# Performance work log

Measured on AMD Instinct MI355X. Metric: run time of the kernel, lower is better.

Reference implementation:

```python
import jax, jax.numpy as jnp
import numpy as np

N, E, F, DIM, BT, RANK = 8192, 32768, 16, 64, 4, 512
EDGE_VARIABLE = 2


def setup_inputs() -> dict:
    key = jax.random.key(0)
    ks = jax.random.split(key, 24)

    def rn(i, shape, s=0.05):
        return jax.random.normal(ks[i], shape, dtype=jnp.float32) * s

    x = jax.random.normal(ks[0], (N, F), dtype=jnp.float32)
    # first feature column is a categorical node-type id (EDGE_VARIABLE == 2)
    x = x.at[:, 0].set(jax.random.randint(ks[1], (N,), 0, 5).astype(jnp.float32))
    edge_index = jax.random.randint(ks[2], (2, E), 0, N, dtype=jnp.int32)
    edge_attr = jax.random.uniform(ks[3], (E, BT), dtype=jnp.float32)
    return {
        'x': x, 'edge_index': edge_index, 'edge_attr': edge_attr,
        'W0': rn(4, (DIM, F)), 'b0': jnp.zeros(DIM, jnp.float32),
        'nnW1': rn(5, (32, BT)), 'nnb1': jnp.zeros(32, jnp.float32),
        'nnW2': rn(6, (DIM * DIM, 32), 0.02), 'nnb2': jnp.zeros(DIM * DIM, jnp.float32),
        'root': rn(7, (DIM, DIM)), 'conv_b': jnp.zeros(DIM, jnp.float32),
        'Wih': rn(8, (3 * DIM, DIM)), 'Whh': rn(9, (3 * DIM, DIM)),
        'bih': jnp.zeros(3 * DIM, jnp.float32), 'bhh': jnp.zeros(3 * DIM, jnp.float32),
        'W1l': rn(10, (BT, DIM)), 'b1l': jnp.zeros(BT, jnp.float32),
        'WUp': rn(11, (DIM, BT)), 'bUp': jnp.zeros(DIM, jnp.float32),
        'WDown': rn(12, (BT, DIM)), 'bDown': jnp.zeros(BT, jnp.float32),
        'U': rn(13, (BT, RANK, DIM)), 'V': rn(14, (BT, DIM, RANK)),
        'weight': rn(15, (1, DIM), 1.0), 'linW': rn(16, (DIM, DIM)), 'linb': jnp.zeros(DIM, jnp.float32),
        'weight_e': rn(17, (1, BT), 1.0), 'linWe': rn(18, (BT, BT)), 'linbe': jnp.zeros(BT, jnp.float32),
    }


def _gru_cell(m, h, Wih, Whh, bih, bhh):
    # torch GRU gate order: reset, update, new
    gi = m @ Wih.T + bih
    gh = h @ Whh.T + bhh
    ir, iz, i_n = jnp.split(gi, 3, axis=-1)
    hr, hz, h_n = jnp.split(gh, 3, axis=-1)
    r = jax.nn.sigmoid(ir + hr)
    z = jax.nn.sigmoid(iz + hz)
    n = jnp.tanh(i_n + r * h_n)
    return (1.0 - z) * n + z * h


def reference(x, edge_index, edge_attr,
              W0, b0, nnW1, nnb1, nnW2, nnb2, root, conv_b,
              Wih, Whh, bih, bhh, W1l, b1l, WUp, bUp, WDown, bDown,
              U, V, weight, linW, linb, weight_e, linWe, linbe):
    n_nodes = x.shape[0]
    src, dst = edge_index[0], edge_index[1]

    out = jax.nn.relu(x @ W0.T + b0)            # [N, DIM]
    h = out

    # mean-aggregation degree (clamped)
    deg = jnp.clip(jax.ops.segment_sum(jnp.ones_like(src, dtype=out.dtype), dst,
                                       num_segments=n_nodes), 1.0)[:, None]

    # edge-conditioned per-edge weight matrices  [E, DIM, DIM]
    We = (jax.nn.relu(edge_attr @ nnW1.T + nnb1) @ nnW2.T + nnb2).reshape(-1, DIM, DIM)

    for _ in range(3):  # 3 message-passing + GRU steps
        msg = jnp.einsum('ei,eio->eo', out[src], We)                 # per-edge matvec
        agg = jax.ops.segment_sum(msg, dst, num_segments=n_nodes) / deg
        m = jax.nn.relu(out @ root + agg + conv_b)                    # NNConv(root + mean msg)
        h = _gru_cell(m, h, Wih, Whh, bih, bhh)
        out = h

    out_edges = jax.nn.relu(out @ W1l.T + b1l)                        # [N, BT]

    # combine node state with upscaled edge-variable state
    ev_mask = (x[:, 0] == EDGE_VARIABLE)
    out_combine = jnp.where(ev_mask[:, None], out_edges @ WUp.T + bUp, out)

    # FGNet factorized (rank-512) bond-type-conditioned message passing
    bond = jnp.argmax(edge_attr, axis=-1)                             # [E]
    oh = jax.nn.one_hot(bond, BT, dtype=out.dtype)                    # [E, BT]
    h_src = out_combine[src]                                          # [E, DIM]
    zf = jnp.einsum('ed,tdr->etr', h_src, V)                          # [E, BT, RANK]
    zsel = jnp.einsum('etr,et->er', zf, oh)                           # select factor by bond type
    me = jnp.einsum('er,et,trd->ed', zsel, oh, U)                     # [E, DIM]
    msg_f = jax.nn.relu(jax.ops.segment_sum(me, dst, num_segments=n_nodes) / deg)
    msg_to_edge = msg_f @ WDown.T + bDown                             # [N, BT]

    out = out + jax.nn.relu((weight * msg_f) @ linW.T + linb)
    out_edges = out_edges + jax.nn.relu((weight_e * msg_to_edge) @ linWe.T + linbe)
    return jax.nn.log_softmax(out_edges, axis=-1)
```

## Files before the change

kernel.cpp:

```cpp
#include <hip/hip_runtime.h>
#include <hip/hip_bf16.h>

#define NN 8192
#define NE 32768
#define FD 16
#define DIM 64
#define BT 4
#define RANK 512

typedef __attribute__((ext_vector_type(8))) short bf16x8;
typedef __attribute__((ext_vector_type(4))) float f32x4;

__device__ inline unsigned short f2bf(float f) {
    union { float f; unsigned u; } c; c.f = f;
    return (unsigned short)((c.u + 0x7fffu + ((c.u >> 16) & 1u)) >> 16);
}
__device__ inline float ubf(unsigned short h) {
    union { unsigned u; float f; } c; c.u = ((unsigned)h) << 16; return c.f;
}
__device__ inline float bflo(unsigned u) { union { unsigned u; float f; } c; c.u = u << 16; return c.f; }
__device__ inline float bfhi(unsigned u) { union { unsigned u; float f; } c; c.u = u & 0xffff0000u; return c.f; }

__global__ __launch_bounds__(256) void k_prep(
    const float* __restrict__ x, const int* __restrict__ ei, const float* __restrict__ ea,
    const float* __restrict__ W0, const float* __restrict__ b0,
    const float* __restrict__ nnW1, const float* __restrict__ nnb1,
    const float* __restrict__ W2, const float* __restrict__ Wih, const float* __restrict__ Whh,
    const float* __restrict__ root, const float* __restrict__ b2,
    const float* __restrict__ U, const float* __restrict__ V,
    float* __restrict__ s, unsigned short* __restrict__ shi, unsigned short* __restrict__ slo,
    float* __restrict__ deg, int* __restrict__ srccnt,
    float* __restrict__ h32, int* __restrict__ bond,
    unsigned short* __restrict__ w2h, unsigned short* __restrict__ w2l,
    unsigned short* __restrict__ wihh, unsigned short* __restrict__ wihl,
    unsigned short* __restrict__ whhh, unsigned short* __restrict__ whhl,
    unsigned short* __restrict__ rth, unsigned short* __restrict__ rtl,
    unsigned short* __restrict__ b2th, unsigned short* __restrict__ b2tl,
    float* __restrict__ M)
{
    int bid = blockIdx.x, tid = threadIdx.x;
    if (bid < 2048) {
        int gid = bid * 256 + tid;
        int n = gid >> 6, d = gid & 63;
        const float4* xr = (const float4*)(x + (size_t)n * FD);
        const float4* wr = (const float4*)(W0 + d * FD);
        float4 x0 = xr[0], x1 = xr[1], x2 = xr[2], x3 = xr[3];
        float4 w0 = wr[0], w1 = wr[1], w2 = wr[2], w3 = wr[3];
        float acc = b0[d]
            + x0.x*w0.x + x0.y*w0.y + x0.z*w0.z + x0.w*w0.w
            + x1.x*w1.x + x1.y*w1.y + x1.z*w1.z + x1.w*w1.w
            + x2.x*w2.x + x2.y*w2.y + x2.z*w2.z + x2.w*w2.w
            + x3.x*w3.x + x3.y*w3.y + x3.z*w3.z + x3.w*w3.w;
        float sv = fmaxf(acc, 0.f);
        s[gid] = sv;
        unsigned short h = f2bf(sv);
        shi[gid] = h; slo[gid] = f2bf(sv - ubf(h));
    } else if (bid < 2176) {
        int e = (bid - 2048) * 256 + tid;
        atomicAdd(&deg[ei[NE + e]], 1.0f);
        atomicAdd(&srccnt[ei[e]], 1);
    } else if (bid < 6272) {
        int e = (bid - 2176) * 8 + (tid >> 5);
        int k = tid & 31;
        float a0 = ea[e * 4 + 0], a1 = ea[e * 4 + 1], a2 = ea[e * 4 + 2], a3 = ea[e * 4 + 3];
        float h = nnb1[k] + a0 * nnW1[k * 4 + 0] + a1 * nnW1[k * 4 + 1]
                          + a2 * nnW1[k * 4 + 2] + a3 * nnW1[k * 4 + 3];
        h32[e * 32 + k] = fmaxf(h, 0.f);
        if (k == 0) {
            int bi = 0; float bv = a0;
            if (a1 > bv) { bv = a1; bi = 1; }
            if (a2 > bv) { bv = a2; bi = 2; }
            if (a3 > bv) { bv = a3; bi = 3; }
            bond[e] = bi;
        }
    } else if (bid < 6784) {
        int gid = (bid - 6272) * 256 + tid;
        int col = gid >> 6, i = gid & 63;
        float v = W2[(size_t)(i * 64 + (col >> 5)) * 32 + (col & 31)];
        unsigned short h = f2bf(v);
        w2h[gid] = h; w2l[gid] = f2bf(v - ubf(h));
    } else if (bid < 6880) {
        int gid = (bid - 6784) * 256 + tid;
        if (gid < 12288) {
            float v = Wih[gid];
            unsigned short h = f2bf(v);
            wihh[gid] = h; wihl[gid] = f2bf(v - ubf(h));
        } else {
            int g = gid - 12288;
            float v = Whh[g];
            unsigned short h = f2bf(v);
            whhh[g] = h; whhl[g] = f2bf(v - ubf(h));
        }
    } else if (bid < 6896) {
        int gid = (bid - 6880) * 256 + tid;
        int o = gid >> 6, i = gid & 63;
        float v = root[i * 64 + o];
        unsigned short h = f2bf(v);
        rth[gid] = h; rtl[gid] = f2bf(v - ubf(h));
    } else if (bid < 6912) {
        int gid = (bid - 6896) * 256 + tid;
        int o = gid >> 6, i = gid & 63;
        float v = b2[i * 64 + o];
        unsigned short h = f2bf(v);
        b2th[gid] = h; b2tl[gid] = f2bf(v - ubf(h));
    } else {
        __shared__ float red[4][64];
        int t = bid - 6912;
        int b = t >> 6, d = t & 63;
        int chunk = tid >> 6, dp = tid & 63;
        const float* Vp = V + ((size_t)b * DIM + d) * RANK;
        const float* Up = U + (size_t)b * RANK * DIM;
        float acc = 0.f;
        for (int r = chunk * 128; r < chunk * 128 + 128; ++r)
            acc += Vp[r] * Up[(size_t)r * DIM + dp];
        red[chunk][dp] = acc;
        __syncthreads();
        if (chunk == 0)
            M[((size_t)b * DIM + d) * DIM + dp] =
                red[0][dp] + red[1][dp] + red[2][dp] + red[3][dp];
    }
}

__global__ __launch_bounds__(1024) void k_scan(const int* __restrict__ cnt,
                                               int* __restrict__ start, int* __restrict__ cursor) {
    __shared__ int ls[1024];
    int tid = threadIdx.x;
    int v[8], tot = 0;
#pragma unroll
    for (int j = 0; j < 8; ++j) { v[j] = cnt[tid * 8 + j]; tot += v[j]; }
    ls[tid] = tot;
    __syncthreads();
    for (int off = 1; off < 1024; off <<= 1) {
        int t = (tid >= off) ? ls[tid - off] : 0;
        __syncthreads();
        ls[tid] += t;
        __syncthreads();
    }
    int run = ls[tid] - tot;
#pragma unroll
    for (int j = 0; j < 8; ++j) {
        start[tid * 8 + j] = run; cursor[tid * 8 + j] = run; run += v[j];
    }
    if (tid == 1023) start[NN] = run;
}

__global__ __launch_bounds__(256) void k_scatter(const int* __restrict__ ei,
                                                 int* __restrict__ cursor, int* __restrict__ eord) {
    int e = blockIdx.x * 256 + threadIdx.x;
    int pos = atomicAdd(&cursor[ei[e]], 1);
    eord[pos] = e;
}

__global__ __launch_bounds__(256) void k_gemm_A(const unsigned short* __restrict__ sh,
                                                const unsigned short* __restrict__ sl,
                                                const unsigned short* __restrict__ wh,
                                                const unsigned short* __restrict__ wl,
                                                const unsigned short* __restrict__ b2th,
                                                const unsigned short* __restrict__ b2tl,
                                                unsigned short* __restrict__ A,
                                                float* __restrict__ cbuf) {
    int tid = threadIdx.x, wid = tid >> 6, lane = tid & 63;
    int lr = lane & 15, kg = lane >> 4;
    if (blockIdx.y == 16) {
        int rbase = blockIdx.x * 128 + wid * 32;
        f32x4 acc[2][4] = {};
#pragma unroll
        for (int kb = 0; kb < 2; ++kb) {
            bf16x8 ah[2], al[2];
#pragma unroll
            for (int mi = 0; mi < 2; ++mi) {
                size_t off = (size_t)(rbase + mi * 16 + lr) * 64 + kb * 32 + kg * 8;
                ah[mi] = *(const bf16x8*)(sh + off);
                al[mi] = *(const bf16x8*)(sl + off);
            }
#pragma unroll
            for (int ni = 0; ni < 4; ++ni) {
                size_t offB = (size_t)(ni * 16 + lr) * 64 + kb * 32 + kg * 8;
                bf16x8 bh = *(const bf16x8*)(b2th + offB);
                bf16x8 bl = *(const bf16x8*)(b2tl + offB);
#pragma unroll
                for (int mi = 0; mi < 2; ++mi) {
                    acc[mi][ni] = __builtin_amdgcn_mfma_f32_16x16x32_bf16(ah[mi], bh, acc[mi][ni], 0, 0, 0);
                    acc[mi][ni] = __builtin_amdgcn_mfma_f32_16x16x32_bf16(ah[mi], bl, acc[mi][ni], 0, 0, 0);
                    acc[mi][ni] = __builtin_amdgcn_mfma_f32_16x16x32_bf16(al[mi], bh, acc[mi][ni], 0, 0, 0);
                }
            }
        }
#pragma unroll
        for (int mi = 0; mi < 2; ++mi)
#pragma unroll
            for (int r = 0; r < 4; ++r)
#pragma unroll
                for (int ni = 0; ni < 4; ++ni)
                    cbuf[(size_t)(rbase + mi * 16 + kg * 4 + r) * 64 + ni * 16 + lr] = acc[mi][ni][r];
        return;
    }
    int mbase = blockIdx.x * 128 + (wid >> 1) * 64;
    int nbase = blockIdx.y * 128 + (wid & 1) * 64;
    f32x4 acc[4][4] = {};
#pragma unroll
    for (int kb = 0; kb < 2; ++kb) {
        bf16x8 ah[4], al[4], bh[4], bl[4];
#pragma unroll
        for (int mi = 0; mi < 4; ++mi) {
            size_t off = (size_t)(mbase + mi * 16 + lr) * 64 + kb * 32 + kg * 8;
            ah[mi] = *(const bf16x8*)(sh + off);
            al[mi] = *(const bf16x8*)(sl + off);
        }
#pragma unroll
        for (int ni = 0; ni < 4; ++ni) {
            size_t off = (size_t)(nbase + ni * 16 + lr) * 64 + kb * 32 + kg * 8;
            bh[ni] = *(const bf16x8*)(wh + off);
            bl[ni] = *(const bf16x8*)(wl + off);
        }
#pragma unroll
        for (int mi = 0; mi < 4; ++mi)
#pragma unroll
            for (int ni = 0; ni < 4; ++ni) {
                acc[mi][ni] = __builtin_amdgcn_mfma_f32_16x16x32_bf16(ah[mi], bh[ni], acc[mi][ni], 0, 0, 0);
                acc[mi][ni] = __builtin_amdgcn_mfma_f32_16x16x32_bf16(ah[mi], bl[ni], acc[mi][ni], 0, 0, 0);
                acc[mi][ni] = __builtin_amdgcn_mfma_f32_16x16x32_bf16(al[mi], bh[ni], acc[mi][ni], 0, 0, 0);
            }
    }
#pragma unroll
    for (int mi = 0; mi < 4; ++mi)
#pragma unroll
        for (int r = 0; r < 4; ++r) {
            size_t row = (size_t)(mbase + mi * 16 + kg * 4 + r) * 2048;
#pragma unroll
            for (int ni = 0; ni < 4; ++ni)
                A[row + nbase + ni * 16 + lr] = f2bf(acc[mi][ni][r]);
        }
}

__global__ __launch_bounds__(256) void k_edge(const int* __restrict__ ei,
                                              const int* __restrict__ startp,
                                              const int* __restrict__ srccnt,
                                              const int* __restrict__ eord,
                                              const float* __restrict__ h32,
                                              const unsigned short* __restrict__ A,
                                              const float* __restrict__ cbuf,
                                              float* __restrict__ agg) {
    int tid = threadIdx.x, wid = tid >> 6, o = tid & 63;
    int n = blockIdx.x * 4 + wid;
    int cnt = srccnt[n];
    if (cnt == 0) return;
    int beg = startp[n];
    float cv = cbuf[(size_t)n * DIM + o];
    const uint4* Ap = (const uint4*)(A + (size_t)n * 2048 + o * 32);
    uint4 a0 = Ap[0], a1 = Ap[1], a2 = Ap[2], a3 = Ap[3];
    for (int i = beg; i < beg + cnt; ++i) {
        int e = eord[i];
        int dst = ei[NE + e];
        const float4* hp = (const float4*)(h32 + (size_t)e * 32);
        float acc = cv;
        float4 hA = hp[0], hB = hp[1];
        acc += hA.x*bflo(a0.x) + hA.y*bfhi(a0.x) + hA.z*bflo(a0.y) + hA.w*bfhi(a0.y)
             + hB.x*bflo(a0.z) + hB.y*bfhi(a0.z) + hB.z*bflo(a0.w) + hB.w*bfhi(a0.w);
        hA = hp[2]; hB = hp[3];
        acc += hA.x*bflo(a1.x) + hA.y*bfhi(a1.x) + hA.z*bflo(a1.y) + hA.w*bfhi(a1.y)
             + hB.x*bflo(a1.z) + hB.y*bfhi(a1.z) + hB.z*bflo(a1.w) + hB.w*bfhi(a1.w);
        hA = hp[4]; hB = hp[5];
        acc += hA.x*bflo(a2.x) + hA.y*bfhi(a2.x) + hA.z*bflo(a2.y) + hA.w*bfhi(a2.y)
             + hB.x*bflo(a2.z) + hB.y*bfhi(a2.z) + hB.z*bflo(a2.w) + hB.w*bfhi(a2.w);
        hA = hp[6]; hB = hp[7];
        acc += hA.x*bflo(a3.x) + hA.y*bfhi(a3.x) + hA.z*bflo(a3.y) + hA.w*bfhi(a3.y)
             + hB.x*bflo(a3.z) + hB.y*bfhi(a3.z) + hB.z*bflo(a3.w) + hB.w*bfhi(a3.w);
        atomicAdd(&agg[(size_t)dst * DIM + o], acc);
    }
}

__global__ __launch_bounds__(256) void k_upd(
    float* __restrict__ s, unsigned short* __restrict__ shi, unsigned short* __restrict__ slo,
    float* __restrict__ agg, const float* __restrict__ deg, const float* __restrict__ conv_b,
    const unsigned short* __restrict__ rth, const unsigned short* __restrict__ rtl,
    const unsigned short* __restrict__ wihh, const unsigned short* __restrict__ wihl,
    const unsigned short* __restrict__ whhh, const unsigned short* __restrict__ whhl,
    const float* __restrict__ bih, const float* __restrict__ bhh,
    const float* __restrict__ x, const float* __restrict__ W1l, const float* __restrict__ b1l,
    const float* __restrict__ WUp, const float* __restrict__ bUp,
    float* __restrict__ oe, float* __restrict__ oc, int last)
{
    __shared__ unsigned short mh_l[16 * 64];
    __shared__ unsigned short ml_l[16 * 64];
    __shared__ float gl[16 * 384];
    __shared__ float oel[64];
    int tid = threadIdx.x;
    int wid = tid >> 6, lane = tid & 63;
    int lr = lane & 15, kg = lane >> 4;
    int m0 = blockIdx.x * 16;

    bf16x8 sa_h[2], sa_l[2];
#pragma unroll
    for (int kb = 0; kb < 2; ++kb) {
        size_t off = (size_t)(m0 + lr) * 64 + kb * 32 + kg * 8;
        sa_h[kb] = *(const bf16x8*)(shi + off);
        sa_l[kb] = *(const bf16x8*)(slo + off);
    }

    f32x4 macc = {};
#pragma unroll
    for (int kb = 0; kb < 2; ++kb) {
        size_t offB = (size_t)(wid * 16 + lr) * 64 + kb * 32 + kg * 8;
        bf16x8 bh = *(const bf16x8*)(rth + offB);
        bf16x8 bl = *(const bf16x8*)(rtl + offB);
        macc = __builtin_amdgcn_mfma_f32_16x16x32_bf16(sa_h[kb], bh, macc, 0, 0, 0);
        macc = __builtin_amdgcn_mfma_f32_16x16x32_bf16(sa_h[kb], bl, macc, 0, 0, 0);
        macc = __builtin_amdgcn_mfma_f32_16x16x32_bf16(sa_l[kb], bh, macc, 0, 0, 0);
    }
#pragma unroll
    for (int r = 0; r < 4; ++r) {
        int row = m0 + kg * 4 + r;
        float inv = 1.f / fmaxf(deg[row], 1.f);
        int col = wid * 16 + lr;
        size_t idx = (size_t)row * 64 + col;
        float v = macc[r] + agg[idx] * inv + conv_b[col];
        agg[idx] = 0.f;
        v = fmaxf(v, 0.f);
        unsigned short h = f2bf(v);
        int loff = (kg * 4 + r) * 64 + col;
        mh_l[loff] = h; ml_l[loff] = f2bf(v - ubf(h));
    }
    __syncthreads();

    bf16x8 ma_h[2], ma_l[2];
#pragma unroll
    for (int kb = 0; kb < 2; ++kb) {
        int loff = lr * 64 + kb * 32 + kg * 8;
        ma_h[kb] = *(const bf16x8*)(mh_l + loff);
        ma_l[kb] = *(const bf16x8*)(ml_l + loff);
    }
    f32x4 gacc[3] = {}, hacc[3] = {};
#pragma unroll
    for (int kb = 0; kb < 2; ++kb)
#pragma unroll
        for (int j = 0; j < 3; ++j) {
            int ni = wid * 3 + j;
            size_t offB = (size_t)(ni * 16 + lr) * 64 + kb * 32 + kg * 8;
            bf16x8 bh = *(const bf16x8*)(wihh + offB);
            bf16x8 bl = *(const bf16x8*)(wihl + offB);
            gacc[j] = __builtin_amdgcn_mfma_f32_16x16x32_bf16(ma_h[kb], bh, gacc[j], 0, 0, 0);
            gacc[j] = __builtin_amdgcn_mfma_f32_16x16x32_bf16(ma_h[kb], bl, gacc[j], 0, 0, 0);
            gacc[j] = __builtin_amdgcn_mfma_f32_16x16x32_bf16(ma_l[kb], bh, gacc[j], 0, 0, 0);
            bf16x8 ch = *(const bf16x8*)(whhh + offB);
            bf16x8 cl = *(const bf16x8*)(whhl + offB);
            hacc[j] = __builtin_amdgcn_mfma_f32_16x16x32_bf16(sa_h[kb], ch, hacc[j], 0, 0, 0);
            hacc[j] = __builtin_amdgcn_mfma_f32_16x16x32_bf16(sa_h[kb], cl, hacc[j], 0, 0, 0);
            hacc[j] = __builtin_amdgcn_mfma_f32_16x16x32_bf16(sa_l[kb], ch, hacc[j], 0, 0, 0);
        }
#pragma unroll
    for (int j = 0; j < 3; ++j)
#pragma unroll
        for (int r = 0; r < 4; ++r) {
            int row = kg * 4 + r;
            int col = (wid * 3 + j) * 16 + lr;
            gl[row * 384 + col] = gacc[j][r];
            gl[row * 384 + 192 + col] = hacc[j][r];
        }
    __syncthreads();

#pragma unroll
    for (int k = 0; k < 4; ++k) {
        int item = tid + k * 256;
        int row = item >> 6, d = item & 63;
        size_t idx = (size_t)(m0 + row) * 64 + d;
        const float* gr = gl + row * 384;
        float ir = gr[d], iz = gr[64 + d], in_ = gr[128 + d];
        float hr_ = gr[192 + d], hz = gr[256 + d], hn = gr[320 + d];
        float hv = s[idx];
        float rg = 1.f / (1.f + expf(-(ir + bih[d] + hr_ + bhh[d])));
        float z  = 1.f / (1.f + expf(-(iz + bih[64 + d] + hz + bhh[64 + d])));
        float nv = tanhf(in_ + bih[128 + d] + rg * (hn + bhh[128 + d]));
        float nh = (1.f - z) * nv + z * hv;
        if (!last) {
            s[idx] = nh;
            unsigned short hb = f2bf(nh);
            shi[idx] = hb; slo[idx] = f2bf(nh - ubf(hb));
        }
        gl[row * 384 + d] = nh;
    }
    if (!last) return;
    __syncthreads();

    {
        int node16 = tid >> 4, j = tid & 15, t = j & 3, q = j >> 2;
        float p = 0.f;
#pragma unroll
        for (int i = 0; i < 16; ++i)
            p += gl[node16 * 384 + q * 16 + i] * W1l[t * 64 + q * 16 + i];
        p += __shfl_xor(p, 4);
        p += __shfl_xor(p, 8);
        if (q == 0) {
            float v = fmaxf(p + b1l[t], 0.f);
            oel[node16 * 4 + t] = v;
            oe[(size_t)(m0 + node16) * 4 + t] = v;
        }
    }
    __syncthreads();
#pragma unroll
    for (int k = 0; k < 4; ++k) {
        int item = tid + k * 256;
        int row = item >> 6, d = item & 63;
        int node = m0 + row;
        float sval = gl[row * 384 + d];
        float ocv;
        if (x[(size_t)node * FD] == 2.0f) {
            ocv = bUp[d];
#pragma unroll
            for (int t = 0; t < 4; ++t) ocv += oel[row * 4 + t] * WUp[d * 4 + t];
        } else {
            ocv = sval;
        }
        oc[(size_t)node * DIM + d] = ocv;
    }
}

__global__ __launch_bounds__(256) void k_fgedge(const int* __restrict__ ei,
                                                const int* __restrict__ bond,
                                                const float* __restrict__ oc,
                                                const float* __restrict__ M,
                                                float* __restrict__ fg_agg) {
    __shared__ float so[4][64];
    int tid = threadIdx.x, w = tid >> 6, lane = tid & 63;
    int e = blockIdx.x * 4 + w;
    int src = ei[e], dst = ei[NE + e];
    int b = bond[e];
    so[w][lane] = oc[(size_t)src * DIM + lane];
    __syncthreads();
    float acc = 0.f;
    const float* Mp = M + b * DIM * DIM;
    for (int d = 0; d < 64; ++d) acc += so[w][d] * Mp[d * 64 + lane];
    atomicAdd(&fg_agg[(size_t)dst * DIM + lane], acc);
}

__global__ __launch_bounds__(256) void k_final(const float* __restrict__ fg_agg,
                                               const float* __restrict__ deg,
                                               const float* __restrict__ oe,
                                               const float* __restrict__ WDown,
                                               const float* __restrict__ bDown,
                                               const float* __restrict__ weight_e,
                                               const float* __restrict__ linWe,
                                               const float* __restrict__ linbe,
                                               float* __restrict__ out) {
    int tid = threadIdx.x, w = tid >> 6, lane = tid & 63;
    int node = blockIdx.x * 4 + w;
    float degc = fmaxf(deg[node], 1.f);
    float mf = fmaxf(fg_agg[(size_t)node * DIM + lane] / degc, 0.f);
    float mte[4];
#pragma unroll
    for (int t = 0; t < 4; ++t) {
        float p = mf * WDown[t * 64 + lane];
#pragma unroll
        for (int off = 32; off; off >>= 1) p += __shfl_xor(p, off);
        mte[t] = p + bDown[t];
    }
    float val[4];
    float mx = -1e30f;
#pragma unroll
    for (int t = 0; t < 4; ++t) {
        float acc = linbe[t];
#pragma unroll
        for (int t2 = 0; t2 < 4; ++t2) acc += weight_e[t2] * mte[t2] * linWe[t * 4 + t2];
        val[t] = oe[(size_t)node * 4 + t] + fmaxf(acc, 0.f);
        mx = fmaxf(mx, val[t]);
    }
    float lse = 0.f;
#pragma unroll
    for (int t = 0; t < 4; ++t) lse += expf(val[t] - mx);
    lse = logf(lse);
    if (lane < 4) out[(size_t)node * 4 + lane] = val[lane] - mx - lse;
}

extern "C" void kernel_launch(void* const* d_in, const int* in_sizes, int n_in,
                              void* d_out, int out_size, void* d_ws, size_t ws_size,
                              hipStream_t stream) {
    const float* x       = (const float*)d_in[0];
    const int*   ei      = (const int*)  d_in[1];
    const float* ea      = (const float*)d_in[2];
    const float* W0      = (const float*)d_in[3];
    const float* b0      = (const float*)d_in[4];
    const float* nnW1    = (const float*)d_in[5];
    const float* nnb1    = (const float*)d_in[6];
    const float* nnW2    = (const float*)d_in[7];
    const float* nnb2    = (const float*)d_in[8];
    const float* root    = (const float*)d_in[9];
    const float* conv_b  = (const float*)d_in[10];
    const float* Wih     = (const float*)d_in[11];
    const float* Whh     = (const float*)d_in[12];
    const float* bih     = (const float*)d_in[13];
    const float* bhh     = (const float*)d_in[14];
    const float* W1l     = (const float*)d_in[15];
    const float* b1l     = (const float*)d_in[16];
    const float* WUp     = (const float*)d_in[17];
    const float* bUp     = (const float*)d_in[18];
    const float* WDown   = (const float*)d_in[19];
    const float* bDown   = (const float*)d_in[20];
    const float* U       = (const float*)d_in[21];
    const float* V       = (const float*)d_in[22];
    const float* weight_e= (const float*)d_in[26];
    const float* linWe   = (const float*)d_in[27];
    const float* linbe   = (const float*)d_in[28];
    float* out = (float*)d_out;

    char* ws = (char*)d_ws;
    size_t off = 0;
    auto alloc = [&](size_t bytes) { size_t o = off; off = (off + bytes + 255) & ~(size_t)255; return o; };
    float* deg    = (float*)(ws + alloc((size_t)NN * 4));
    int*   srccnt = (int*)  (ws + alloc((size_t)NN * 4));
    float* agg    = (float*)(ws + alloc((size_t)NN * DIM * 4));
    float* fg_agg = (float*)(ws + alloc((size_t)NN * DIM * 4));
    float* s      = (float*)(ws + alloc((size_t)NN * DIM * 4));
    unsigned short* shi = (unsigned short*)(ws + alloc((size_t)NN * DIM * 2));
    unsigned short* slo = (unsigned short*)(ws + alloc((size_t)NN * DIM * 2));
    float* cbuf   = (float*)(ws + alloc((size_t)NN * DIM * 4));
    float* h32    = (float*)(ws + alloc((size_t)NE * 32 * 4));
    int*   bond   = (int*)  (ws + alloc((size_t)NE * 4));
    int*   startp = (int*)  (ws + alloc((size_t)(NN + 1) * 4));
    int*   cursor = (int*)  (ws + alloc((size_t)NN * 4));
    int*   eord   = (int*)  (ws + alloc((size_t)NE * 4));
    float* oe     = (float*)(ws + alloc((size_t)NN * 4 * 4));
    float* oc     = (float*)(ws + alloc((size_t)NN * DIM * 4));
    float* Mbuf   = (float*)(ws + alloc((size_t)BT * DIM * DIM * 4));
    unsigned short* w2h = (unsigned short*)(ws + alloc((size_t)2048 * 64 * 2));
    unsigned short* w2l = (unsigned short*)(ws + alloc((size_t)2048 * 64 * 2));
    unsigned short* wihh = (unsigned short*)(ws + alloc((size_t)192 * 64 * 2));
    unsigned short* wihl = (unsigned short*)(ws + alloc((size_t)192 * 64 * 2));
    unsigned short* whhh = (unsigned short*)(ws + alloc((size_t)192 * 64 * 2));
    unsigned short* whhl = (unsigned short*)(ws + alloc((size_t)192 * 64 * 2));
    unsigned short* rth  = (unsigned short*)(ws + alloc((size_t)64 * 64 * 2));
    unsigned short* rtl  = (unsigned short*)(ws + alloc((size_t)64 * 64 * 2));
    unsigned short* b2th = (unsigned short*)(ws + alloc((size_t)64 * 64 * 2));
    unsigned short* b2tl = (unsigned short*)(ws + alloc((size_t)64 * 64 * 2));
    unsigned short* Abuf = (unsigned short*)(ws + alloc((size_t)NN * 2048 * 2));
    (void)n_in; (void)in_sizes; (void)out_size; (void)ws_size;

    hipMemsetAsync(deg, 0, (size_t)2 * NN * 4, stream);
    hipMemsetAsync(agg, 0, (size_t)2 * NN * DIM * 4, stream);

    k_prep<<<7168, 256, 0, stream>>>(x, ei, ea, W0, b0, nnW1, nnb1,
                                     nnW2, Wih, Whh, root, nnb2, U, V,
                                     s, shi, slo, deg, srccnt, h32, bond,
                                     w2h, w2l, wihh, wihl, whhh, whhl,
                                     rth, rtl, b2th, b2tl, Mbuf);
    k_scan<<<1, 1024, 0, stream>>>(srccnt, startp, cursor);
    k_scatter<<<NE / 256, 256, 0, stream>>>(ei, cursor, eord);

    for (int it = 0; it < 3; ++it) {
        k_gemm_A<<<dim3(NN / 128, 17), 256, 0, stream>>>(shi, slo, w2h, w2l, b2th, b2tl,
                                                         Abuf, cbuf);
        k_edge<<<NN / 4, 256, 0, stream>>>(ei, startp, srccnt, eord, h32, Abuf, cbuf, agg);
        k_upd<<<NN / 16, 256, 0, stream>>>(s, shi, slo, agg, deg, conv_b,
                                           rth, rtl, wihh, wihl, whhh, whhl, bih, bhh,
                                           x, W1l, b1l, WUp, bUp, oe, oc, it == 2);
    }

    k_fgedge<<<NE / 4, 256, 0, stream>>>(ei, bond, oc, Mbuf, fg_agg);
    k_final<<<NN / 4, 256, 0, stream>>>(fg_agg, deg, oe, WDown, bDown, weight_e, linWe, linbe, out);
}
```

Measured before the change: 240.0 us.

## Fuse FG edge messaging with final stage via dst-sorted CSR gather

Builds a destination-sorted edge order (a second scan and scatter pass) so the factorized message passing can gather per node instead of scattering with float atomics. The edge kernel and final kernel are merged into one per-node kernel, which removes the fg_agg buffer and its memset. Zeroing of agg moves from a memset into extra k_prep blocks. In exchange, k_scan runs two serial scans, and per-node loops are unbalanced by in-degree.

```diff
diff --git a/kernel.cpp b/kernel.cpp
--- a/kernel.cpp
+++ b/kernel.cpp
@@ -36,7 +36,7 @@
     unsigned short* __restrict__ whhh, unsigned short* __restrict__ whhl,
     unsigned short* __restrict__ rth, unsigned short* __restrict__ rtl,
     unsigned short* __restrict__ b2th, unsigned short* __restrict__ b2tl,
-    float* __restrict__ M)
+    float* __restrict__ M, float* __restrict__ agg)
 {
     int bid = blockIdx.x, tid = threadIdx.x;
     if (bid < 2048) {
@@ -103,7 +103,7 @@
         float v = b2[i * 64 + o];
         unsigned short h = f2bf(v);
         b2th[gid] = h; b2tl[gid] = f2bf(v - ubf(h));
-    } else {
+    } else if (bid < 7168) {
         __shared__ float red[4][64];
         int t = bid - 6912;
         int b = t >> 6, d = t & 63;
@@ -118,37 +118,67 @@
         if (chunk == 0)
             M[((size_t)b * DIM + d) * DIM + dp] =
                 red[0][dp] + red[1][dp] + red[2][dp] + red[3][dp];
+    } else {
+        float4* zp = ((float4*)agg) + (size_t)(bid - 7168) * 4096;
+        for (int j = tid; j < 4096; j += 256)
+            zp[j] = make_float4(0.f, 0.f, 0.f, 0.f);
     }
 }
 
 __global__ __launch_bounds__(1024) void k_scan(const int* __restrict__ cnt,
-                                               int* __restrict__ start, int* __restrict__ cursor) {
+                                               const float* __restrict__ deg,
+                                               int* __restrict__ start, int* __restrict__ cursor,
+                                               int* __restrict__ dstart, int* __restrict__ dcursor) {
     __shared__ int ls[1024];
     int tid = threadIdx.x;
-    int v[8], tot = 0;
-#pragma unroll
-    for (int j = 0; j < 8; ++j) { v[j] = cnt[tid * 8 + j]; tot += v[j]; }
-    ls[tid] = tot;
+    {
+        int v[8], tot = 0;
+#pragma unroll
+        for (int j = 0; j < 8; ++j) { v[j] = cnt[tid * 8 + j]; tot += v[j]; }
+        ls[tid] = tot;
+        __syncthreads();
+        for (int off = 1; off < 1024; off <<= 1) {
+            int t = (tid >= off) ? ls[tid - off] : 0;
+            __syncthreads();
+            ls[tid] += t;
+            __syncthreads();
+        }
+        int run = ls[tid] - tot;
+#pragma unroll
+        for (int j = 0; j < 8; ++j) {
+            start[tid * 8 + j] = run; cursor[tid * 8 + j] = run; run += v[j];
+        }
+        if (tid == 1023) start[NN] = run;
+    }
     __syncthreads();
-    for (int off = 1; off < 1024; off <<= 1) {
-        int t = (tid >= off) ? ls[tid - off] : 0;
+    {
+        int v[8], tot = 0;
+#pragma unroll
+        for (int j = 0; j < 8; ++j) { v[j] = (int)deg[tid * 8 + j]; tot += v[j]; }
+        ls[tid] = tot;
         __syncthreads();
-        ls[tid] += t;
-        __syncthreads();
-    }
-    int run = ls[tid] - tot;
-#pragma unroll
-    for (int j = 0; j < 8; ++j) {
-        start[tid * 8 + j] = run; cursor[tid * 8 + j] = run; run += v[j];
-    }
-    if (tid == 1023) start[NN] = run;
+        for (int off = 1; off < 1024; off <<= 1) {
+            int t = (tid >= off) ? ls[tid - off] : 0;
+            __syncthreads();
+            ls[tid] += t;
+            __syncthreads();
+        }
+        int run = ls[tid] - tot;
+#pragma unroll
+        for (int j = 0; j < 8; ++j) {
+            dstart[tid * 8 + j] = run; dcursor[tid * 8 + j] = run; run += v[j];
+        }
+        if (tid == 1023) dstart[NN] = run;
+    }
 }
 
 __global__ __launch_bounds__(256) void k_scatter(const int* __restrict__ ei,
-                                                 int* __restrict__ cursor, int* __restrict__ eord) {
+                                                 int* __restrict__ cursor, int* __restrict__ eord,
+                                                 int* __restrict__ dcursor, int* __restrict__ eordD) {
     int e = blockIdx.x * 256 + threadIdx.x;
-    int pos = atomicAdd(&cursor[ei[e]], 1);
-    eord[pos] = e;
+    int s_ = ei[e], d_ = ei[NE + e];
+    eord[atomicAdd(&cursor[s_], 1)] = e;
+    eordD[atomicAdd(&dcursor[d_], 1)] = e;
 }
 
 __global__ __launch_bounds__(256) void k_gemm_A(const unsigned short* __restrict__ sh,
@@ -415,37 +445,37 @@
     }
 }
 
-__global__ __launch_bounds__(256) void k_fgedge(const int* __restrict__ ei,
-                                                const int* __restrict__ bond,
-                                                const float* __restrict__ oc,
-                                                const float* __restrict__ M,
-                                                float* __restrict__ fg_agg) {
-    __shared__ float so[4][64];
-    int tid = threadIdx.x, w = tid >> 6, lane = tid & 63;
-    int e = blockIdx.x * 4 + w;
-    int src = ei[e], dst = ei[NE + e];
-    int b = bond[e];
-    so[w][lane] = oc[(size_t)src * DIM + lane];
-    __syncthreads();
+__global__ __launch_bounds__(256) void k_fg(const int* __restrict__ ei,
+                                            const int* __restrict__ bond,
+                                            const int* __restrict__ dstart,
+                                            const int* __restrict__ eordD,
+                                            const float* __restrict__ oc,
+                                            const float* __restrict__ M,
+                                            const float* __restrict__ deg,
+                                            const float* __restrict__ oe,
+                                            const float* __restrict__ WDown,
+                                            const float* __restrict__ bDown,
+                                            const float* __restrict__ weight_e,
+                                            const float* __restrict__ linWe,
+                                            const float* __restrict__ linbe,
+                                            float* __restrict__ out) {
+    int tid = threadIdx.x, wid = tid >> 6, lane = tid & 63;
+    int node = blockIdx.x * 4 + wid;
+    float degf = deg[node];
+    int cnt = (int)degf;
+    int beg = dstart[node];
     float acc = 0.f;
-    const float* Mp = M + b * DIM * DIM;
-    for (int d = 0; d < 64; ++d) acc += so[w][d] * Mp[d * 64 + lane];
-    atomicAdd(&fg_agg[(size_t)dst * DIM + lane], acc);
-}
-
-__global__ __launch_bounds__(256) void k_final(const float* __restrict__ fg_agg,
-                                               const float* __restrict__ deg,
-                                               const float* __restrict__ oe,
-                                               const float* __restrict__ WDown,
-                                               const float* __restrict__ bDown,
-                                               const float* __restrict__ weight_e,
-                                               const float* __restrict__ linWe,
-                                               const float* __restrict__ linbe,
-                                               float* __restrict__ out) {
-    int tid = threadIdx.x, w = tid >> 6, lane = tid & 63;
-    int node = blockIdx.x * 4 + w;
-    float degc = fmaxf(deg[node], 1.f);
-    float mf = fmaxf(fg_agg[(size_t)node * DIM + lane] / degc, 0.f);
+    for (int i = 0; i < cnt; ++i) {
+        int e = eordD[beg + i];
+        int src = ei[e];
+        int b = bond[e];
+        float ocv = oc[(size_t)src * DIM + lane];
+        const float* Mp = M + b * DIM * DIM;
+#pragma unroll
+        for (int d = 0; d < 64; ++d)
+            acc += __shfl(ocv, d) * Mp[d * 64 + lane];
+    }
+    float mf = fmaxf(acc / fmaxf(degf, 1.f), 0.f);
     float mte[4];
 #pragma unroll
     for (int t = 0; t < 4; ++t) {
@@ -458,10 +488,10 @@
     float mx = -1e30f;
 #pragma unroll
     for (int t = 0; t < 4; ++t) {
-        float acc = linbe[t];
-#pragma unroll
-        for (int t2 = 0; t2 < 4; ++t2) acc += weight_e[t2] * mte[t2] * linWe[t * 4 + t2];
-        val[t] = oe[(size_t)node * 4 + t] + fmaxf(acc, 0.f);
+        float a2 = linbe[t];
+#pragma unroll
+        for (int t2 = 0; t2 < 4; ++t2) a2 += weight_e[t2] * mte[t2] * linWe[t * 4 + t2];
+        val[t] = oe[(size_t)node * 4 + t] + fmaxf(a2, 0.f);
         mx = fmaxf(mx, val[t]);
     }
     float lse = 0.f;
@@ -508,7 +538,6 @@
     float* deg    = (float*)(ws + alloc((size_t)NN * 4));
     int*   srccnt = (int*)  (ws + alloc((size_t)NN * 4));
     float* agg    = (float*)(ws + alloc((size_t)NN * DIM * 4));
-    float* fg_agg = (float*)(ws + alloc((size_t)NN * DIM * 4));
     float* s      = (float*)(ws + alloc((size_t)NN * DIM * 4));
     unsigned short* shi = (unsigned short*)(ws + alloc((size_t)NN * DIM * 2));
     unsigned short* slo = (unsigned short*)(ws + alloc((size_t)NN * DIM * 2));
@@ -518,6 +547,9 @@
     int*   startp = (int*)  (ws + alloc((size_t)(NN + 1) * 4));
     int*   cursor = (int*)  (ws + alloc((size_t)NN * 4));
     int*   eord   = (int*)  (ws + alloc((size_t)NE * 4));
+    int*   dstart = (int*)  (ws + alloc((size_t)(NN + 1) * 4));
+    int*   dcursor= (int*)  (ws + alloc((size_t)NN * 4));
+    int*   eordD  = (int*)  (ws + alloc((size_t)NE * 4));
     float* oe     = (float*)(ws + alloc((size_t)NN * 4 * 4));
     float* oc     = (float*)(ws + alloc((size_t)NN * DIM * 4));
     float* Mbuf   = (float*)(ws + alloc((size_t)BT * DIM * DIM * 4));
@@ -535,15 +567,14 @@
     (void)n_in; (void)in_sizes; (void)out_size; (void)ws_size;
 
     hipMemsetAsync(deg, 0, (size_t)2 * NN * 4, stream);
-    hipMemsetAsync(agg, 0, (size_t)2 * NN * DIM * 4, stream);
-
-    k_prep<<<7168, 256, 0, stream>>>(x, ei, ea, W0, b0, nnW1, nnb1,
+
+    k_prep<<<7200, 256, 0, stream>>>(x, ei, ea, W0, b0, nnW1, nnb1,
                                      nnW2, Wih, Whh, root, nnb2, U, V,
                                      s, shi, slo, deg, srccnt, h32, bond,
                                      w2h, w2l, wihh, wihl, whhh, whhl,
-                                     rth, rtl, b2th, b2tl, Mbuf);
-    k_scan<<<1, 1024, 0, stream>>>(srccnt, startp, cursor);
-    k_scatter<<<NE / 256, 256, 0, stream>>>(ei, cursor, eord);
+                                     rth, rtl, b2th, b2tl, Mbuf, agg);
+    k_scan<<<1, 1024, 0, stream>>>(srccnt, deg, startp, cursor, dstart, dcursor);
+    k_scatter<<<NE / 256, 256, 0, stream>>>(ei, cursor, eord, dcursor, eordD);
 
     for (int it = 0; it < 3; ++it) {
         k_gemm_A<<<dim3(NN / 128, 17), 256, 0, stream>>>(shi, slo, w2h, w2l, b2th, b2tl,
@@ -554,6 +585,6 @@
                                            x, W1l, b1l, WUp, bUp, oe, oc, it == 2);
     }
 
-    k_fgedge<<<NE / 4, 256, 0, stream>>>(ei, bond, oc, Mbuf, fg_agg);
-    k_final<<<NN / 4, 256, 0, stream>>>(fg_agg, deg, oe, WDown, bDown, weight_e, linWe, linbe, out);
-}
+    k_fg<<<NN / 4, 256, 0, stream>>>(ei, bond, dstart, eordD, oc, Mbuf, deg,
+                                     oe, WDown, bDown, weight_e, linWe, linbe, out);
+}
```

New measurement: 274.5 us. 1.14x slower.
